# Kernel tuning notes

Measured on AMD Instinct MI355X. Metric: run time of the kernel, lower is better.

Reference implementation:

```python
import jax, jax.numpy as jnp
import numpy as np

TOP_K = 2  # num_experts_per_token


def setup_inputs() -> dict:
    key = jax.random.key(0)
    ks = jax.random.split(key, 6)
    B, S, H, F, E = 4, 2048, 1024, 4096, 8  # F = 2 * intermediate_size
    scale = 0.02
    x = jax.random.normal(ks[0], (B, S, H), dtype=jnp.float32)
    gate_w = jax.random.normal(ks[1], (E, H), dtype=jnp.float32) * scale
    w1 = jax.random.normal(ks[2], (E, H, F), dtype=jnp.float32) * scale
    b1 = jnp.zeros((E, F), dtype=jnp.float32)
    w2 = jax.random.normal(ks[3], (E, F, H), dtype=jnp.float32) * scale
    b2 = jnp.zeros((E, H), dtype=jnp.float32)
    return {"x": x, "gate_w": gate_w, "w1": w1, "b1": b1, "w2": w2, "b2": b2}


def reference(x, gate_w, w1, b1, w2, b2):
    # x: [B, S, H]; gate_w: [E, H]; w1: [E, H, F]; b1: [E, F]; w2: [E, F, H]; b2: [E, H]
    E = gate_w.shape[0]
    gate_logits = jnp.einsum('bsh,eh->bse', x, gate_w)
    gate_probs = jax.nn.softmax(gate_logits, axis=-1)
    top_v, top_i = jax.lax.top_k(gate_probs, TOP_K)  # [B, S, K]
    # Combine weight per expert: w[b,s,e] = sum_k top_v[b,s,k] * (top_i[b,s,k] == e)
    onehot = jax.nn.one_hot(top_i, E, dtype=x.dtype)          # [B, S, K, E]
    comb_w = jnp.einsum('bsk,bske->bse', top_v, onehot)       # [B, S, E]
    out = jnp.zeros_like(x)
    for e in range(E):  # small fixed expert loop
        h = jax.nn.silu(jnp.einsum('bsh,hf->bsf', x, w1[e]) + b1[e])
        y = jnp.einsum('bsf,fh->bsh', h, w2[e]) + b2[e]
        out = out + y * comb_w[..., e:e + 1]
    return out
```

## Files before the change

kernel.cpp:

```cpp
#include <hip/hip_runtime.h>
#include <stdint.h>

#define T_TOK 8192
#define HDIM  1024
#define FDIM  4096
#define NEXP  8
#define BT    256
#define RCAP  (2*T_TOK + NEXP*256)
#define LDSB  65536

typedef short  short8  __attribute__((ext_vector_type(8)));
typedef unsigned short ushort8 __attribute__((ext_vector_type(8)));
typedef float  f32x4   __attribute__((ext_vector_type(4)));

#define MFMA __builtin_amdgcn_mfma_f32_16x16x32_bf16

__device__ __forceinline__ unsigned short f2bf(float f) {
  unsigned u = __float_as_uint(f);
  u += 0x7fffu + ((u >> 16) & 1u);
  return (unsigned short)(u >> 16);
}
__device__ __forceinline__ float bf2f(unsigned short u) {
  return __uint_as_float((unsigned)u << 16);
}

__device__ __forceinline__ void gload16(const void* g, void* l) {
  __builtin_amdgcn_global_load_lds(
      (const __attribute__((address_space(1))) void*)g,
      (__attribute__((address_space(3))) void*)l, 16, 0, 0);
}

__global__ __launch_bounds__(256) void k_transp_cvt(const float* __restrict__ in,
                                                    unsigned short* __restrict__ out,
                                                    int K, int N) {
  __shared__ unsigned short s[64][72];
  const float* ine = in + (size_t)blockIdx.z * K * N;
  unsigned short* oute = out + (size_t)blockIdx.z * K * N;
  int k0 = blockIdx.y * 64, n0 = blockIdx.x * 64;
  int t = threadIdx.x;
  int kr = t >> 4, nc = (t & 15) * 4;
#pragma unroll
  for (int it = 0; it < 4; ++it) {
    int k = it * 16 + kr;
    float4 v = *(const float4*)(ine + (size_t)(k0 + k) * N + n0 + nc);
    ushort4 u = make_ushort4(f2bf(v.x), f2bf(v.y), f2bf(v.z), f2bf(v.w));
    *(ushort4*)(&s[k][nc]) = u;
  }
  __syncthreads();
  int nr = t >> 3, kc = (t & 7) * 8;
#pragma unroll
  for (int v = 0; v < 2; ++v) {
    int n = v * 32 + nr;
    ushort8 o;
#pragma unroll
    for (int j = 0; j < 8; ++j) o[j] = s[kc + j][n];
    *(ushort8*)(oute + (size_t)(n0 + n) * K + k0 + kc) = o;
  }
}

__global__ void k_gate(const float* __restrict__ x, const float* __restrict__ gw,
                       unsigned short* __restrict__ xb,
                       int2* __restrict__ eidx, float2* __restrict__ ewt) {
  int tid = threadIdx.x;
  int lane = tid & 63;
  int t = blockIdx.x * 4 + (tid >> 6);
  const float* xr = x + (size_t)t * HDIM;
  unsigned short* xbr = xb + (size_t)t * HDIM;
  float acc[NEXP];
#pragma unroll
  for (int e = 0; e < NEXP; e++) acc[e] = 0.f;
#pragma unroll
  for (int i = 0; i < 4; i++) {
    int idx = i * 256 + lane * 4;
    float4 xv = *(const float4*)(xr + idx);
    *(ushort4*)(xbr + idx) = make_ushort4(f2bf(xv.x), f2bf(xv.y), f2bf(xv.z), f2bf(xv.w));
#pragma unroll
    for (int e = 0; e < NEXP; e++) {
      float4 gv = *(const float4*)(gw + e * HDIM + idx);
      acc[e] += xv.x * gv.x + xv.y * gv.y + xv.z * gv.z + xv.w * gv.w;
    }
  }
#pragma unroll
  for (int e = 0; e < NEXP; e++) {
    acc[e] += __shfl_xor(acc[e], 32);
    acc[e] += __shfl_xor(acc[e], 16);
    acc[e] += __shfl_xor(acc[e], 8);
    acc[e] += __shfl_xor(acc[e], 4);
    acc[e] += __shfl_xor(acc[e], 2);
    acc[e] += __shfl_xor(acc[e], 1);
  }
  float m = acc[0];
#pragma unroll
  for (int e = 1; e < NEXP; e++) m = fmaxf(m, acc[e]);
  float p[NEXP]; float s = 0.f;
#pragma unroll
  for (int e = 0; e < NEXP; e++) { p[e] = expf(acc[e] - m); s += p[e]; }
  float inv = 1.f / s;
#pragma unroll
  for (int e = 0; e < NEXP; e++) p[e] *= inv;
  int b0 = 0; float v0 = p[0];
#pragma unroll
  for (int e = 1; e < NEXP; e++) if (p[e] > v0) { v0 = p[e]; b0 = e; }
  int b1i = (b0 == 0) ? 1 : 0; float v1 = p[b1i];
#pragma unroll
  for (int e = 0; e < NEXP; e++) if (e != b0 && p[e] > v1) { v1 = p[e]; b1i = e; }
  if (lane == 0) { eidx[t] = make_int2(b0, b1i); ewt[t] = make_float2(v0, v1); }
}

__global__ __launch_bounds__(1024) void k_compact(const int2* __restrict__ eidx,
                          int* __restrict__ list_tok, int* __restrict__ counts) {
  int e = blockIdx.x;
  int tid = threadIdx.x, lane = tid & 63, wid = tid >> 6;
  __shared__ int sbase;
  __shared__ int wcnt[16];
  if (tid == 0) sbase = 0;
  __syncthreads();
  for (int c = 0; c < T_TOK; c += 1024) {
    int t = c + tid;
    int2 ei = eidx[t];
    bool sel = (ei.x == e) || (ei.y == e);
    unsigned long long b = __ballot(sel);
    if (lane == 0) wcnt[wid] = __popcll(b);
    __syncthreads();
    int pre = sbase;
    for (int w = 0; w < wid; w++) pre += wcnt[w];
    int pos = pre + __popcll(b & ((1ull << lane) - 1ull));
    if (sel) list_tok[e * T_TOK + pos] = t;
    __syncthreads();
    if (tid == 0) {
      int tot = 0;
      for (int w = 0; w < 16; w++) tot += wcnt[w];
      sbase += tot;
    }
    __syncthreads();
  }
  if (tid == 0) counts[e] = sbase;
}

__global__ void k_offsets(const int* __restrict__ counts, int* __restrict__ off_pad) {
  if (threadIdx.x == 0) {
    int o = 0;
    off_pad[0] = 0;
    for (int e = 0; e < NEXP; e++) {
      o += ((counts[e] + BT - 1) / BT) * BT;
      off_pad[e + 1] = o;
    }
  }
}

__global__ void k_invert(const int* __restrict__ list_tok, const int* __restrict__ counts,
                         const int* __restrict__ off_pad, const int2* __restrict__ eidx,
                         int2* __restrict__ tok2slot) {
  int e = blockIdx.y;
  int p = blockIdx.x * 256 + threadIdx.x;
  if (p < counts[e]) {
    int t = list_tok[e * T_TOK + p];
    int slot = off_pad[e] + p;
    if (eidx[t].x == e) tok2slot[t].x = slot;
    else                tok2slot[t].y = slot;
  }
}

#define CFENCE asm volatile("" ::: "memory")

#define STAGE_A(u_, v_) { \
    char* lb_ = smem + (((v_)&1) ? LDSB : 0) + (u_)*16384; \
    gload16(gA[u_][0] + (size_t)(v_)*128, lb_ + dst0); \
    gload16(gA[u_][1] + (size_t)(v_)*128, lb_ + dst1); }
#define STAGE_B(u_, v_) { \
    char* lb_ = smem + (((v_)&1) ? LDSB : 0) + 32768 + (u_)*16384; \
    gload16(gB[u_][0] + (size_t)(v_)*128, lb_ + dst0); \
    gload16(gB[u_][1] + (size_t)(v_)*128, lb_ + dst1); }

#define PHASE2(M0_, M1_, M2_, M3_, STAGE_STMT, TAIL_STMT) { \
    short8 a0l = *(const short8*)(pA0 + (M0_)*2048), a0h = *(const short8*)(pA1 + (M0_)*2048); \
    short8 a1l = *(const short8*)(pA0 + (M1_)*2048), a1h = *(const short8*)(pA1 + (M1_)*2048); \
    short8 a2l = *(const short8*)(pA0 + (M2_)*2048), a2h = *(const short8*)(pA1 + (M2_)*2048); \
    short8 a3l = *(const short8*)(pA0 + (M3_)*2048), a3h = *(const short8*)(pA1 + (M3_)*2048); \
    STAGE_STMT; \
    CFENCE; \
    __builtin_amdgcn_s_barrier(); \
    CFENCE; \
    acc[M0_][0] = MFMA(a0l, b00, acc[M0_][0], 0,0,0); \
    acc[M0_][1] = MFMA(a0l, b10, acc[M0_][1], 0,0,0); \
    acc[M0_][2] = MFMA(a0l, b20, acc[M0_][2], 0,0,0); \
    acc[M0_][3] = MFMA(a0l, b30, acc[M0_][3], 0,0,0); \
    acc[M1_][0] = MFMA(a1l, b00, acc[M1_][0], 0,0,0); \
    acc[M1_][1] = MFMA(a1l, b10, acc[M1_][1], 0,0,0); \
    acc[M1_][2] = MFMA(a1l, b20, acc[M1_][2], 0,0,0); \
    acc[M1_][3] = MFMA(a1l, b30, acc[M1_][3], 0,0,0); \
    acc[M2_][0] = MFMA(a2l, b00, acc[M2_][0], 0,0,0); \
    acc[M2_][1] = MFMA(a2l, b10, acc[M2_][1], 0,0,0); \
    acc[M2_][2] = MFMA(a2l, b20, acc[M2_][2], 0,0,0); \
    acc[M2_][3] = MFMA(a2l, b30, acc[M2_][3], 0,0,0); \
    acc[M3_][0] = MFMA(a3l, b00, acc[M3_][0], 0,0,0); \
    acc[M3_][1] = MFMA(a3l, b10, acc[M3_][1], 0,0,0); \
    acc[M3_][2] = MFMA(a3l, b20, acc[M3_][2], 0,0,0); \
    acc[M3_][3] = MFMA(a3l, b30, acc[M3_][3], 0,0,0); \
    acc[M0_][0] = MFMA(a0h, b01, acc[M0_][0], 0,0,0); \
    acc[M0_][1] = MFMA(a0h, b11, acc[M0_][1], 0,0,0); \
    acc[M0_][2] = MFMA(a0h, b21, acc[M0_][2], 0,0,0); \
    acc[M0_][3] = MFMA(a0h, b31, acc[M0_][3], 0,0,0); \
    acc[M1_][0] = MFMA(a1h, b01, acc[M1_][0], 0,0,0); \
    acc[M1_][1] = MFMA(a1h, b11, acc[M1_][1], 0,0,0); \
    acc[M1_][2] = MFMA(a1h, b21, acc[M1_][2], 0,0,0); \
    acc[M1_][3] = MFMA(a1h, b31, acc[M1_][3], 0,0,0); \
    acc[M2_][0] = MFMA(a2h, b01, acc[M2_][0], 0,0,0); \
    acc[M2_][1] = MFMA(a2h, b11, acc[M2_][1], 0,0,0); \
    acc[M2_][2] = MFMA(a2h, b21, acc[M2_][2], 0,0,0); \
    acc[M2_][3] = MFMA(a2h, b31, acc[M2_][3], 0,0,0); \
    acc[M3_][0] = MFMA(a3h, b01, acc[M3_][0], 0,0,0); \
    acc[M3_][1] = MFMA(a3h, b11, acc[M3_][1], 0,0,0); \
    acc[M3_][2] = MFMA(a3h, b21, acc[M3_][2], 0,0,0); \
    acc[M3_][3] = MFMA(a3h, b31, acc[M3_][3], 0,0,0); \
    TAIL_STMT; \
    CFENCE; \
    __builtin_amdgcn_s_barrier(); \
    CFENCE; }

#define READ_B4 \
    short8 b00 = *(const short8*)(pB0),        b01 = *(const short8*)(pB1); \
    short8 b10 = *(const short8*)(pB0 + 2048), b11 = *(const short8*)(pB1 + 2048); \
    short8 b20 = *(const short8*)(pB0 + 4096), b21 = *(const short8*)(pB1 + 4096); \
    short8 b30 = *(const short8*)(pB0 + 6144), b31 = *(const short8*)(pB1 + 6144);

#define GEMM_TILE_LOOP(NT) \
  STAGE_A(0,0); STAGE_A(1,0); STAGE_B(0,0); STAGE_B(1,0); STAGE_B(0,1); STAGE_B(1,1); \
  asm volatile("s_waitcnt vmcnt(4)" ::: "memory"); \
  __builtin_amdgcn_s_barrier(); \
  CFENCE; \
  for (int v = 0; v < (NT); ++v) { \
    const char* bufb = smem + ((v&1) ? LDSB : 0); \
    const char* pA0 = bufb + wm * 16384 + aoff0; \
    const char* pA1 = bufb + wm * 16384 + aoff1; \
    const char* pB0 = bufb + 32768 + (wn >> 1) * 16384 + boff0; \
    const char* pB1 = bufb + 32768 + (wn >> 1) * 16384 + boff1; \
    READ_B4; \
    PHASE2(0, 1, 2, 3, { if (v+1 < (NT)) { STAGE_A(0, v+1); STAGE_A(1, v+1); } }, {}); \
    PHASE2(4, 5, 6, 7, { if (v+2 < (NT)) { STAGE_B(0, v+2); STAGE_B(1, v+2); } }, { \
      if (v+2 < (NT))      { asm volatile("s_waitcnt vmcnt(4)" ::: "memory"); } \
      else if (v+1 < (NT)) { asm volatile("s_waitcnt vmcnt(0)" ::: "memory"); } }); \
  }

__global__ __launch_bounds__(512, 2) void k_gemm1(
    const unsigned short* __restrict__ xb, const unsigned short* __restrict__ w1t,
    const float* __restrict__ b1, const int* __restrict__ list_tok,
    const int* __restrict__ counts, const int* __restrict__ off_pad,
    unsigned short* __restrict__ h) {
  extern __shared__ char smem[];
  int wl = (blockIdx.x & 7) * 144 + (blockIdx.x >> 3);
  int r0 = (wl >> 4) * BT;
  int n0 = (wl & 15) * BT;
  if (r0 >= off_pad[NEXP]) return;
  int e = 0;
#pragma unroll
  for (int i = 0; i < NEXP; ++i) if (r0 >= off_pad[i + 1]) e = i + 1;
  int base = off_pad[e], cnt = counts[e];

  int t = threadIdx.x, l = t & 63, w = t >> 6;
  int wm = w >> 2, wn = w & 3;
  int lr = l & 15, g16 = (l >> 4) * 16;
  int swz = (lr & 7) << 4;
  int aoff0 = lr * 128 + (g16 ^ swz);
  int aoff1 = lr * 128 + ((64 + g16) ^ swz);
  int boff0 = (wn & 1) * 8192 + aoff0;
  int boff1 = (wn & 1) * 8192 + aoff1;

  int dst0 = t * 16, dst1 = t * 16 + 8192;
  int srow = t >> 3;
  int skb = (((t & 7) ^ ((t >> 3) & 7)) << 4);
  const char* gA[2][2];
  const char* gB[2][2];
#pragma unroll
  for (int u = 0; u < 2; ++u)
#pragma unroll
    for (int j = 0; j < 2; ++j) {
      int row = u * 128 + srow + 64 * j;
      int se = r0 - base + row;
      int tok = (se < cnt) ? list_tok[e * T_TOK + se] : 0;
      gA[u][j] = (const char*)(xb + (size_t)tok * HDIM) + skb;
      gB[u][j] = (const char*)(w1t + (size_t)e * FDIM * HDIM + (size_t)(n0 + row) * HDIM) + skb;
    }

  f32x4 acc[8][4];
#pragma unroll
  for (int m = 0; m < 8; ++m)
#pragma unroll
    for (int n = 0; n < 4; ++n) acc[m][n] = (f32x4){0.f, 0.f, 0.f, 0.f};

  GEMM_TILE_LOOP(HDIM / 64);

  const float* b1e = b1 + (size_t)e * FDIM + n0;
  unsigned short* Cs = (unsigned short*)smem;
  int lh = l >> 4, lh4 = lh * 4;
  int cswz = lh << 4;
#pragma unroll
  for (int n = 0; n < 4; ++n) {
    int col = wn * 64 + n * 16 + lr;
    int colX = col ^ cswz;
    float bv = b1e[col];
#pragma unroll
    for (int m = 0; m < 8; ++m) {
      int row = wm * 128 + m * 16 + lh4;
#pragma unroll
      for (int i = 0; i < 4; ++i) {
        float vv = acc[m][n][i] + bv;
        float sg = __builtin_amdgcn_rcpf(1.f + __expf(-vv));
        Cs[(size_t)(row + i) * BT + colX] = f2bf(vv * sg);
      }
    }
  }
  __syncthreads();
#pragma unroll
  for (int s = 0; s < 16; ++s) {
    int lin = s * 512 + t;
    int row = lin >> 5, c8 = (lin & 31) * 8;
    int c8X = c8 ^ (((row >> 2) & 3) << 4);
    *(ushort8*)(h + (size_t)(r0 + row) * FDIM + n0 + c8) = *(const ushort8*)(Cs + (size_t)row * BT + c8X);
  }
}

__global__ __launch_bounds__(512, 2) void k_gemm2(
    const unsigned short* __restrict__ h, const unsigned short* __restrict__ w2t,
    const float* __restrict__ b2, const int* __restrict__ off_pad,
    unsigned short* __restrict__ ypartA, unsigned short* __restrict__ ypartB) {
  extern __shared__ char smem[];
  int wl = (blockIdx.x & 7) * 72 + (blockIdx.x >> 3);
  int mB = wl >> 3, rem = wl & 7;
  int r0 = mB * BT;
  int n0 = (rem >> 1) * BT;
  int z  = rem & 1;
  if (r0 >= off_pad[NEXP]) return;
  int e = 0;
#pragma unroll
  for (int i = 0; i < NEXP; ++i) if (r0 >= off_pad[i + 1]) e = i + 1;

  int t = threadIdx.x, l = t & 63, w = t >> 6;
  int wm = w >> 2, wn = w & 3;
  int lr = l & 15, g16 = (l >> 4) * 16;
  int swz = (lr & 7) << 4;
  int aoff0 = lr * 128 + (g16 ^ swz);
  int aoff1 = lr * 128 + ((64 + g16) ^ swz);
  int boff0 = (wn & 1) * 8192 + aoff0;
  int boff1 = (wn & 1) * 8192 + aoff1;

  int dst0 = t * 16, dst1 = t * 16 + 8192;
  int srow = t >> 3;
  int skb = (((t & 7) ^ ((t >> 3) & 7)) << 4);
  const char* gA[2][2];
  const char* gB[2][2];
#pragma unroll
  for (int u = 0; u < 2; ++u)
#pragma unroll
    for (int j = 0; j < 2; ++j) {
      int row = u * 128 + srow + 64 * j;
      gA[u][j] = (const char*)(h + (size_t)(r0 + row) * FDIM + (size_t)z * 2048) + skb;
      gB[u][j] = (const char*)(w2t + (size_t)e * HDIM * FDIM + (size_t)(n0 + row) * FDIM + (size_t)z * 2048) + skb;
    }

  f32x4 acc[8][4];
#pragma unroll
  for (int m = 0; m < 8; ++m)
#pragma unroll
    for (int n = 0; n < 4; ++n) acc[m][n] = (f32x4){0.f, 0.f, 0.f, 0.f};

  GEMM_TILE_LOOP(2048 / 64);

  const float* b2e = b2 + (size_t)e * HDIM + n0;
  unsigned short* yp = z ? ypartB : ypartA;
  unsigned short* Cs = (unsigned short*)smem;
  int lh = l >> 4, lh4 = lh * 4;
  int cswz = lh << 4;
#pragma unroll
  for (int n = 0; n < 4; ++n) {
    int col = wn * 64 + n * 16 + lr;
    int colX = col ^ cswz;
    float bv = (z == 0) ? b2e[col] : 0.f;
#pragma unroll
    for (int m = 0; m < 8; ++m) {
      int row = wm * 128 + m * 16 + lh4;
#pragma unroll
      for (int i = 0; i < 4; ++i)
        Cs[(size_t)(row + i) * BT + colX] = f2bf(acc[m][n][i] + bv);
    }
  }
  __syncthreads();
#pragma unroll
  for (int s = 0; s < 16; ++s) {
    int lin = s * 512 + t;
    int row = lin >> 5, c8 = (lin & 31) * 8;
    int c8X = c8 ^ (((row >> 2) & 3) << 4);
    *(ushort8*)(yp + (size_t)(r0 + row) * HDIM + n0 + c8) = *(const ushort8*)(Cs + (size_t)row * BT + c8X);
  }
}

__global__ void k_reduce(const unsigned short* __restrict__ ypartA,
                         const unsigned short* __restrict__ ypartB,
                         const int2* __restrict__ tok2slot, const float2* __restrict__ ewt,
                         float* __restrict__ out) {
  int idx = blockIdx.x * 256 + threadIdx.x;
  int t = idx >> 7;
  int c8 = (idx & 127) * 8;
  int2 s = tok2slot[t];
  float2 wv = ewt[t];
  ushort8 a0 = *(const ushort8*)(ypartA + (size_t)s.x * HDIM + c8);
  ushort8 a1 = *(const ushort8*)(ypartB + (size_t)s.x * HDIM + c8);
  ushort8 b0 = *(const ushort8*)(ypartA + (size_t)s.y * HDIM + c8);
  ushort8 b1 = *(const ushort8*)(ypartB + (size_t)s.y * HDIM + c8);
  float o[8];
#pragma unroll
  for (int j = 0; j < 8; ++j)
    o[j] = wv.x * (bf2f((unsigned short)a0[j]) + bf2f((unsigned short)a1[j]))
         + wv.y * (bf2f((unsigned short)b0[j]) + bf2f((unsigned short)b1[j]));
  float* op = out + (size_t)t * HDIM + c8;
  *(float4*)op = make_float4(o[0], o[1], o[2], o[3]);
  *(float4*)(op + 4) = make_float4(o[4], o[5], o[6], o[7]);
}

extern "C" void kernel_launch(void* const* d_in, const int* in_sizes, int n_in,
                              void* d_out, int out_size, void* d_ws, size_t ws_size,
                              hipStream_t stream) {
  const float* x  = (const float*)d_in[0];
  const float* gw = (const float*)d_in[1];
  const float* w1 = (const float*)d_in[2];
  const float* b1 = (const float*)d_in[3];
  const float* w2 = (const float*)d_in[4];
  const float* b2 = (const float*)d_in[5];
  float* out = (float*)d_out;

  char* ws = (char*)d_ws;
  size_t off = 0;
  unsigned short* xb = (unsigned short*)(ws + off); off += (size_t)T_TOK * HDIM * 2;
  int2*   eidx = (int2*)(ws + off);   off += (size_t)T_TOK * 8;
  float2* ewt  = (float2*)(ws + off); off += (size_t)T_TOK * 8;
  int2* tok2slot = (int2*)(ws + off); off += (size_t)T_TOK * 8;
  int*  list_tok = (int*)(ws + off);  off += (size_t)NEXP * T_TOK * 4;
  int* counts  = (int*)(ws + off); off += 64;
  int* off_pad = (int*)(ws + off); off += 64;
  off = (off + 255) & ~(size_t)255;
  unsigned short* h      = (unsigned short*)(ws + off); off += (size_t)RCAP * FDIM * 2;
  unsigned short* wT     = (unsigned short*)(ws + off); off += (size_t)NEXP * HDIM * FDIM * 2;
  unsigned short* ypartA = (unsigned short*)(ws + off); off += (size_t)RCAP * HDIM * 2;
  unsigned short* ypartB = (unsigned short*)(ws + off); off += (size_t)RCAP * HDIM * 2;
  if (ws_size < off) return;

  hipFuncSetAttribute((const void*)k_gemm1, hipFuncAttributeMaxDynamicSharedMemorySize, 131072);
  hipFuncSetAttribute((const void*)k_gemm2, hipFuncAttributeMaxDynamicSharedMemorySize, 131072);

  k_gate<<<T_TOK / 4, 256, 0, stream>>>(x, gw, xb, eidx, ewt);
  k_compact<<<NEXP, 1024, 0, stream>>>(eidx, list_tok, counts);
  k_offsets<<<1, 64, 0, stream>>>(counts, off_pad);
  k_invert<<<dim3(T_TOK / 256, NEXP), 256, 0, stream>>>(list_tok, counts, off_pad, eidx, tok2slot);
  k_transp_cvt<<<dim3(FDIM / 64, HDIM / 64, NEXP), 256, 0, stream>>>(w1, wT, HDIM, FDIM);
  k_gemm1<<<8 * 144, 512, 131072, stream>>>(xb, wT, b1, list_tok, counts, off_pad, h);
  k_transp_cvt<<<dim3(HDIM / 64, FDIM / 64, NEXP), 256, 0, stream>>>(w2, wT, FDIM, HDIM);
  k_gemm2<<<8 * 72, 512, 131072, stream>>>(h, wT, b2, off_pad, ypartA, ypartB);
  k_reduce<<<T_TOK * (HDIM / 8) / 256, 256, 0, stream>>>(ypartA, ypartB, tok2slot, ewt, out);
}
```

Baseline: 464.3 us.

## Restructure GEMM main loop into 8 finer phases with setprio and unrolled double buffer

```diff
diff --git a/kernel.cpp b/kernel.cpp
--- a/kernel.cpp
+++ b/kernel.cpp
@@ -172,74 +172,73 @@
     gload16(gB[u_][0] + (size_t)(v_)*128, lb_ + dst0); \
     gload16(gB[u_][1] + (size_t)(v_)*128, lb_ + dst1); }
 
-#define PHASE2(M0_, M1_, M2_, M3_, STAGE_STMT, TAIL_STMT) { \
-    short8 a0l = *(const short8*)(pA0 + (M0_)*2048), a0h = *(const short8*)(pA1 + (M0_)*2048); \
-    short8 a1l = *(const short8*)(pA0 + (M1_)*2048), a1h = *(const short8*)(pA1 + (M1_)*2048); \
-    short8 a2l = *(const short8*)(pA0 + (M2_)*2048), a2h = *(const short8*)(pA1 + (M2_)*2048); \
-    short8 a3l = *(const short8*)(pA0 + (M3_)*2048), a3h = *(const short8*)(pA1 + (M3_)*2048); \
+#define PH_READ_B(PB0_, PB1_) { \
+    b00 = *(const short8*)(PB0_);          b01 = *(const short8*)(PB1_); \
+    b10 = *(const short8*)((PB0_) + 2048); b11 = *(const short8*)((PB1_) + 2048); \
+    b20 = *(const short8*)((PB0_) + 4096); b21 = *(const short8*)((PB1_) + 4096); \
+    b30 = *(const short8*)((PB0_) + 6144); b31 = *(const short8*)((PB1_) + 6144); }
+
+#define PHASE8(Q_, PA0_, PA1_, BSTMT, STAGE_STMT, TAIL_STMT) { \
+    short8 a0l = *(const short8*)((PA0_) + (2*(Q_))*2048); \
+    short8 a0h = *(const short8*)((PA1_) + (2*(Q_))*2048); \
+    short8 a1l = *(const short8*)((PA0_) + (2*(Q_)+1)*2048); \
+    short8 a1h = *(const short8*)((PA1_) + (2*(Q_)+1)*2048); \
+    BSTMT; \
     STAGE_STMT; \
-    CFENCE; \
-    __builtin_amdgcn_s_barrier(); \
-    CFENCE; \
-    acc[M0_][0] = MFMA(a0l, b00, acc[M0_][0], 0,0,0); \
-    acc[M0_][1] = MFMA(a0l, b10, acc[M0_][1], 0,0,0); \
-    acc[M0_][2] = MFMA(a0l, b20, acc[M0_][2], 0,0,0); \
-    acc[M0_][3] = MFMA(a0l, b30, acc[M0_][3], 0,0,0); \
-    acc[M1_][0] = MFMA(a1l, b00, acc[M1_][0], 0,0,0); \
-    acc[M1_][1] = MFMA(a1l, b10, acc[M1_][1], 0,0,0); \
-    acc[M1_][2] = MFMA(a1l, b20, acc[M1_][2], 0,0,0); \
-    acc[M1_][3] = MFMA(a1l, b30, acc[M1_][3], 0,0,0); \
-    acc[M2_][0] = MFMA(a2l, b00, acc[M2_][0], 0,0,0); \
-    acc[M2_][1] = MFMA(a2l, b10, acc[M2_][1], 0,0,0); \
-    acc[M2_][2] = MFMA(a2l, b20, acc[M2_][2], 0,0,0); \
-    acc[M2_][3] = MFMA(a2l, b30, acc[M2_][3], 0,0,0); \
-    acc[M3_][0] = MFMA(a3l, b00, acc[M3_][0], 0,0,0); \
-    acc[M3_][1] = MFMA(a3l, b10, acc[M3_][1], 0,0,0); \
-    acc[M3_][2] = MFMA(a3l, b20, acc[M3_][2], 0,0,0); \
-    acc[M3_][3] = MFMA(a3l, b30, acc[M3_][3], 0,0,0); \
-    acc[M0_][0] = MFMA(a0h, b01, acc[M0_][0], 0,0,0); \
-    acc[M0_][1] = MFMA(a0h, b11, acc[M0_][1], 0,0,0); \
-    acc[M0_][2] = MFMA(a0h, b21, acc[M0_][2], 0,0,0); \
-    acc[M0_][3] = MFMA(a0h, b31, acc[M0_][3], 0,0,0); \
-    acc[M1_][0] = MFMA(a1h, b01, acc[M1_][0], 0,0,0); \
-    acc[M1_][1] = MFMA(a1h, b11, acc[M1_][1], 0,0,0); \
-    acc[M1_][2] = MFMA(a1h, b21, acc[M1_][2], 0,0,0); \
-    acc[M1_][3] = MFMA(a1h, b31, acc[M1_][3], 0,0,0); \
-    acc[M2_][0] = MFMA(a2h, b01, acc[M2_][0], 0,0,0); \
-    acc[M2_][1] = MFMA(a2h, b11, acc[M2_][1], 0,0,0); \
-    acc[M2_][2] = MFMA(a2h, b21, acc[M2_][2], 0,0,0); \
-    acc[M2_][3] = MFMA(a2h, b31, acc[M2_][3], 0,0,0); \
-    acc[M3_][0] = MFMA(a3h, b01, acc[M3_][0], 0,0,0); \
-    acc[M3_][1] = MFMA(a3h, b11, acc[M3_][1], 0,0,0); \
-    acc[M3_][2] = MFMA(a3h, b21, acc[M3_][2], 0,0,0); \
-    acc[M3_][3] = MFMA(a3h, b31, acc[M3_][3], 0,0,0); \
     TAIL_STMT; \
     CFENCE; \
     __builtin_amdgcn_s_barrier(); \
-    CFENCE; }
-
-#define READ_B4 \
-    short8 b00 = *(const short8*)(pB0),        b01 = *(const short8*)(pB1); \
-    short8 b10 = *(const short8*)(pB0 + 2048), b11 = *(const short8*)(pB1 + 2048); \
-    short8 b20 = *(const short8*)(pB0 + 4096), b21 = *(const short8*)(pB1 + 4096); \
-    short8 b30 = *(const short8*)(pB0 + 6144), b31 = *(const short8*)(pB1 + 6144);
+    asm volatile("s_waitcnt lgkmcnt(0)" ::: "memory"); \
+    __builtin_amdgcn_s_setprio(1); \
+    acc[2*(Q_)  ][0] = MFMA(a0l, b00, acc[2*(Q_)  ][0], 0,0,0); \
+    acc[2*(Q_)  ][1] = MFMA(a0l, b10, acc[2*(Q_)  ][1], 0,0,0); \
+    acc[2*(Q_)  ][2] = MFMA(a0l, b20, acc[2*(Q_)  ][2], 0,0,0); \
+    acc[2*(Q_)  ][3] = MFMA(a0l, b30, acc[2*(Q_)  ][3], 0,0,0); \
+    acc[2*(Q_)+1][0] = MFMA(a1l, b00, acc[2*(Q_)+1][0], 0,0,0); \
+    acc[2*(Q_)+1][1] = MFMA(a1l, b10, acc[2*(Q_)+1][1], 0,0,0); \
+    acc[2*(Q_)+1][2] = MFMA(a1l, b20, acc[2*(Q_)+1][2], 0,0,0); \
+    acc[2*(Q_)+1][3] = MFMA(a1l, b30, acc[2*(Q_)+1][3], 0,0,0); \
+    acc[2*(Q_)  ][0] = MFMA(a0h, b01, acc[2*(Q_)  ][0], 0,0,0); \
+    acc[2*(Q_)  ][1] = MFMA(a0h, b11, acc[2*(Q_)  ][1], 0,0,0); \
+    acc[2*(Q_)  ][2] = MFMA(a0h, b21, acc[2*(Q_)  ][2], 0,0,0); \
+    acc[2*(Q_)  ][3] = MFMA(a0h, b31, acc[2*(Q_)  ][3], 0,0,0); \
+    acc[2*(Q_)+1][0] = MFMA(a1h, b01, acc[2*(Q_)+1][0], 0,0,0); \
+    acc[2*(Q_)+1][1] = MFMA(a1h, b11, acc[2*(Q_)+1][1], 0,0,0); \
+    acc[2*(Q_)+1][2] = MFMA(a1h, b21, acc[2*(Q_)+1][2], 0,0,0); \
+    acc[2*(Q_)+1][3] = MFMA(a1h, b31, acc[2*(Q_)+1][3], 0,0,0); \
+    __builtin_amdgcn_s_setprio(0); \
+    CFENCE; \
+    __builtin_amdgcn_s_barrier(); }
 
 #define GEMM_TILE_LOOP(NT) \
   STAGE_A(0,0); STAGE_A(1,0); STAGE_B(0,0); STAGE_B(1,0); STAGE_B(0,1); STAGE_B(1,1); \
   asm volatile("s_waitcnt vmcnt(4)" ::: "memory"); \
   __builtin_amdgcn_s_barrier(); \
   CFENCE; \
-  for (int v = 0; v < (NT); ++v) { \
-    const char* bufb = smem + ((v&1) ? LDSB : 0); \
-    const char* pA0 = bufb + wm * 16384 + aoff0; \
-    const char* pA1 = bufb + wm * 16384 + aoff1; \
-    const char* pB0 = bufb + 32768 + (wn >> 1) * 16384 + boff0; \
-    const char* pB1 = bufb + 32768 + (wn >> 1) * 16384 + boff1; \
-    READ_B4; \
-    PHASE2(0, 1, 2, 3, { if (v+1 < (NT)) { STAGE_A(0, v+1); STAGE_A(1, v+1); } }, {}); \
-    PHASE2(4, 5, 6, 7, { if (v+2 < (NT)) { STAGE_B(0, v+2); STAGE_B(1, v+2); } }, { \
-      if (v+2 < (NT))      { asm volatile("s_waitcnt vmcnt(4)" ::: "memory"); } \
-      else if (v+1 < (NT)) { asm volatile("s_waitcnt vmcnt(0)" ::: "memory"); } }); \
+  { \
+    const char* pA0_0 = smem + wm * 16384 + aoff0; \
+    const char* pA1_0 = smem + wm * 16384 + aoff1; \
+    const char* pB0_0 = smem + 32768 + (wn >> 1) * 16384 + boff0; \
+    const char* pB1_0 = smem + 32768 + (wn >> 1) * 16384 + boff1; \
+    const char* pA0_1 = pA0_0 + LDSB; \
+    const char* pA1_1 = pA1_0 + LDSB; \
+    const char* pB0_1 = pB0_0 + LDSB; \
+    const char* pB1_1 = pB1_0 + LDSB; \
+    short8 b00, b01, b10, b11, b20, b21, b30, b31; \
+    for (int v = 0; v < (NT); v += 2) { \
+      int more = (v + 2 < (NT)); \
+      PHASE8(0, pA0_0, pA1_0, PH_READ_B(pB0_0, pB1_0), STAGE_A(0, v+1), {}); \
+      PHASE8(1, pA0_0, pA1_0, {}, STAGE_A(1, v+1), {}); \
+      PHASE8(2, pA0_0, pA1_0, {}, { if (more) STAGE_B(0, v+2); }, {}); \
+      PHASE8(3, pA0_0, pA1_0, {}, { if (more) STAGE_B(1, v+2); }, \
+             { if (more) { asm volatile("s_waitcnt vmcnt(4)" ::: "memory"); } \
+               else      { asm volatile("s_waitcnt vmcnt(0)" ::: "memory"); } }); \
+      PHASE8(0, pA0_1, pA1_1, PH_READ_B(pB0_1, pB1_1), { if (more) STAGE_A(0, v+2); }, {}); \
+      PHASE8(1, pA0_1, pA1_1, {}, { if (more) STAGE_A(1, v+2); }, {}); \
+      PHASE8(2, pA0_1, pA1_1, {}, { if (more) STAGE_B(0, v+3); }, {}); \
+      PHASE8(3, pA0_1, pA1_1, {}, { if (more) STAGE_B(1, v+3); }, \
+             { if (more) { asm volatile("s_waitcnt vmcnt(4)" ::: "memory"); } }); \
+    } \
   }
 
 __global__ __launch_bounds__(512, 2) void k_gemm1(
```

Result: slower. 482.9 us (+4.0%).
